# Kernel optimization log

Measured on AMD Instinct MI355X. Metric: run time of the kernel, lower is better.

Reference implementation:

```python
import jax, jax.numpy as jnp
import numpy as np

HEADS = 24
HEAD_DIM = 128
HIDDEN = HEADS * HEAD_DIM          # 3072
MLP_DIM = int(HIDDEN * 4.0)        # 12288
EPS = 1e-6


def _layernorm(x, eps=EPS):
    mu = jnp.mean(x, axis=-1, keepdims=True)
    var = jnp.mean(jnp.square(x - mu), axis=-1, keepdims=True)
    return (x - mu) * jax.lax.rsqrt(var + eps)


def _rmsnorm(x, w, eps=EPS):
    var = jnp.mean(jnp.square(x), axis=-1, keepdims=True)
    return x * jax.lax.rsqrt(var + eps) * w


def _apply_rope_transposed(x, freqs_cis):
    # x: [B, S_img, H, Dh]; freqs_cis: [S_img, 2*Dh]
    cos, sin = jnp.split(freqs_cis[:, None, :], 2, axis=-1)  # each [S_img, 1, Dh]
    xr = x.reshape(*x.shape[:-1], -1, 2)                      # interleaved pairs
    x_real, x_imag = xr[..., 0], xr[..., 1]
    x_rot = jnp.stack([-x_imag, x_real], axis=-1).reshape(x.shape)
    return x * cos + x_rot * sin


def setup_inputs() -> dict:
    key = jax.random.key(0)
    ks = jax.random.split(key, 20)
    B, S_IMG, S_TXT = 1, 2048, 256
    s = 0.02
    inp = {
        "hidden_states": jax.random.normal(ks[0], (B, S_IMG, HIDDEN), jnp.float32),
        "encoder_hidden_states": jax.random.normal(ks[1], (B, S_TXT, HIDDEN), jnp.float32),
        "temb": jax.random.normal(ks[2], (B, HIDDEN), jnp.float32),
        "freqs_cis": jax.random.uniform(ks[3], (S_IMG, 2 * HEAD_DIM), jnp.float32),
        # AdaLN: Linear(hidden, 3*hidden)
        "w_norm": jax.random.normal(ks[4], (HIDDEN, 3 * HIDDEN), jnp.float32) * s,
        "b_norm": jnp.zeros((3 * HIDDEN,), jnp.float32),
        # attention projections (bias=True)
        "wq": jax.random.normal(ks[5], (HIDDEN, HIDDEN), jnp.float32) * s,
        "bq": jnp.zeros((HIDDEN,), jnp.float32),
        "wk": jax.random.normal(ks[6], (HIDDEN, HIDDEN), jnp.float32) * s,
        "bk": jnp.zeros((HIDDEN,), jnp.float32),
        "wv": jax.random.normal(ks[7], (HIDDEN, HIDDEN), jnp.float32) * s,
        "bv": jnp.zeros((HIDDEN,), jnp.float32),
        # QK RMSNorm weights over head_dim
        "nq_w": jnp.ones((HEAD_DIM,), jnp.float32),
        "nk_w": jnp.ones((HEAD_DIM,), jnp.float32),
        # parallel MLP branch
        "w_mlp": jax.random.normal(ks[8], (HIDDEN, MLP_DIM), jnp.float32) * s,
        "b_mlp": jnp.zeros((MLP_DIM,), jnp.float32),
        # proj_out: Linear(hidden + mlp_dim, hidden)
        "w_out": jax.random.normal(ks[9], (HIDDEN + MLP_DIM, HIDDEN), jnp.float32) * s,
        "b_out": jnp.zeros((HIDDEN,), jnp.float32),
    }
    return inp


def reference(hidden_states, encoder_hidden_states, temb, freqs_cis,
              w_norm, b_norm, wq, bq, wk, bk, wv, bv, nq_w, nk_w,
              w_mlp, b_mlp, w_out, b_out):
    B = hidden_states.shape[0]
    T = encoder_hidden_states.shape[1]  # text_seq_length

    x = jnp.concatenate([hidden_states, encoder_hidden_states], axis=1)  # [B,S,D]
    residual = x

    # AdaLayerNormZeroSingle
    emb = jax.nn.silu(temb) @ w_norm + b_norm          # [B, 3D]
    emb = emb[:, None, :]                              # [B, 1, 3D]
    shift, scale, gate = jnp.split(emb, 3, axis=-1)    # each [B,1,D]
    nx = _layernorm(x) * (1.0 + scale) + shift         # [B,S,D]

    # parallel MLP branch
    mlp = jax.nn.gelu(nx @ w_mlp + b_mlp, approximate=True)  # [B,S,MLP]

    # attention: q/k/v over full (img+txt) normed sequence
    q = (nx @ wq + bq).reshape(B, -1, HEADS, HEAD_DIM)
    k = (nx @ wk + bk).reshape(B, -1, HEADS, HEAD_DIM)
    v = (nx @ wv + bv).reshape(B, -1, HEADS, HEAD_DIM)
    q = _rmsnorm(q, nq_w)
    k = _rmsnorm(k, nk_w)

    # transposed RoPE on image tokens only
    q = jnp.concatenate([_apply_rope_transposed(q[:, :-T], freqs_cis), q[:, -T:]], axis=1)
    k = jnp.concatenate([_apply_rope_transposed(k[:, :-T], freqs_cis), k[:, -T:]], axis=1)

    # full (non-varlen) scaled dot-product attention
    scores = jnp.einsum("bqhd,bkhd->bhqk", q, k) / np.sqrt(HEAD_DIM).astype(np.float32)
    probs = jax.nn.softmax(scores, axis=-1)
    attn = jnp.einsum("bhqk,bkhd->bqhd", probs, v).reshape(B, -1, HIDDEN)

    # concat attention + mlp, project, gated residual
    h = jnp.concatenate([attn, mlp], axis=2)           # [B,S,D+MLP]
    h = gate * (h @ w_out + b_out) + residual          # [B,S,D]

    return h[:, :-T, :], h[:, -T:, :]
```

## Files before the change

### kernel.cpp

```cpp
#include <hip/hip_runtime.h>
#include <hip/hip_bf16.h>

typedef unsigned short u16;
typedef short s16x8 __attribute__((ext_vector_type(8)));
typedef float f32x4 __attribute__((ext_vector_type(4)));
typedef int   i32x4 __attribute__((ext_vector_type(4)));
typedef int   i32x2 __attribute__((ext_vector_type(2)));
typedef u16   u16x4 __attribute__((ext_vector_type(4)));
typedef unsigned int u32;
typedef u32   u32x2 __attribute__((ext_vector_type(2)));

#define HEADS  24
#define HD     128
#define HIDDEN 3072
#define MLPD   12288
#define NTOK   2304
#define SIMG   2048
#define NEMB   9216
#define CATD   15360
#define QKVD   9216
#define FUSEN  21504
#define LN_EPS 1e-6f
#define MB     9
#define INV127SQ (1.0f/16129.0f)

__device__ __forceinline__ u16 f2us(float f){
  __hip_bfloat16 h = __float2bfloat16(f);
  return *reinterpret_cast<u16*>(&h);
}
__device__ __forceinline__ float us2f(u16 u){
  __hip_bfloat16 h;
  *reinterpret_cast<u16*>(&h) = u;
  return __bfloat162float(h);
}
__device__ __forceinline__ float gelu_tanh(float x){
  float y = 0.7978845608028654f*(x + 0.044715f*x*x*x);
  y = fminf(fmaxf(y, -12.f), 12.f);
  float e = __expf(-2.f*y);
  float t = (1.f - e) / (1.f + e);
  return 0.5f*x*(1.0f + t);
}
__device__ __forceinline__ int q8i(float x, float s){
  int q = __float2int_rn(x*s);
  return max(-127, min(127, q));
}
__device__ __forceinline__ void gload16(const void* g, void* l){
  __builtin_amdgcn_global_load_lds(
      (const __attribute__((address_space(1))) void*)g,
      (__attribute__((address_space(3))) void*)l, 16, 0, 0);
}
#define BAR() do{ asm volatile("":::"memory"); __builtin_amdgcn_s_barrier(); asm volatile("":::"memory"); }while(0)
#define LGKM0() asm volatile("s_waitcnt lgkmcnt(0)":::"memory")
#define VMW_(n) asm volatile("s_waitcnt vmcnt(" #n ")":::"memory")
#define VMW(n) VMW_(n)

__global__ __launch_bounds__(256)
void emb_partial(const float* __restrict__ temb, const float* __restrict__ wn,
                 float* __restrict__ partial)
{
  __shared__ float ls[384];
  int tid = threadIdx.x;
  int kb = blockIdx.y * 384;
  for (int i = tid; i < 384; i += 256){
    float t = temb[kb + i];
    ls[i] = t / (1.0f + __expf(-t));
  }
  __syncthreads();
  int j = blockIdx.x*256 + tid;
  const float* wp = wn + (size_t)kb*NEMB + j;
  float acc = 0.f;
  #pragma unroll 8
  for (int i = 0; i < 384; i++){ acc = fmaf(ls[i], wp[0], acc); wp += NEMB; }
  partial[blockIdx.y*NEMB + j] = acc;
}

__global__ __launch_bounds__(256)
void emb_reduce(const float* __restrict__ partial, const float* __restrict__ bn,
                float* __restrict__ emb)
{
  int j = blockIdx.x*256 + threadIdx.x;
  float s = bn[j];
  #pragma unroll
  for (int r = 0; r < 8; r++) s += partial[r*NEMB + j];
  emb[j] = s;
}

__global__ __launch_bounds__(256)
void ln_mod(const float* __restrict__ hs, const float* __restrict__ ehs,
            const float* __restrict__ emb, char* __restrict__ nx,
            float* __restrict__ arow)
{
  int row = blockIdx.x;
  const float* x = (row < SIMG) ? hs + (size_t)row*HIDDEN
                                : ehs + (size_t)(row - SIMG)*HIDDEN;
  int tid = threadIdx.x;
  float vals[12];
  float s = 0.f, ss = 0.f;
  #pragma unroll
  for (int i = 0; i < 3; i++){
    float4 v = *reinterpret_cast<const float4*>(x + i*1024 + tid*4);
    vals[i*4+0]=v.x; vals[i*4+1]=v.y; vals[i*4+2]=v.z; vals[i*4+3]=v.w;
    s += v.x+v.y+v.z+v.w;
    ss += v.x*v.x + v.y*v.y + v.z*v.z + v.w*v.w;
  }
  #pragma unroll
  for (int d = 1; d < 64; d <<= 1){ s += __shfl_xor(s, d); ss += __shfl_xor(ss, d); }
  __shared__ float red[8];
  if ((tid & 63) == 0){ red[tid>>6] = s; red[4 + (tid>>6)] = ss; }
  __syncthreads();
  s  = red[0]+red[1]+red[2]+red[3];
  ss = red[4]+red[5]+red[6]+red[7];
  float mu = s * (1.0f/HIDDEN);
  float var = ss * (1.0f/HIDDEN) - mu*mu;
  float rs = rsqrtf(var + LN_EPS);

  float mx = 1e-8f;
  #pragma unroll
  for (int i = 0; i < 3; i++){
    int col = i*1024 + tid*4;
    #pragma unroll
    for (int j = 0; j < 4; j++){
      float nv = (vals[i*4+j] - mu) * rs;
      float outv = nv * (1.0f + emb[HIDDEN + col + j]) + emb[col + j];
      vals[i*4+j] = outv;
      mx = fmaxf(mx, fabsf(outv));
    }
  }
  #pragma unroll
  for (int d = 1; d < 64; d <<= 1) mx = fmaxf(mx, __shfl_xor(mx, d));
  __shared__ float redm[4];
  if ((tid & 63) == 0) redm[tid>>6] = mx;
  __syncthreads();
  mx = fmaxf(fmaxf(redm[0], redm[1]), fmaxf(redm[2], redm[3]));
  if (tid == 0) arow[row] = mx;
  float sq = 127.0f / mx;

  #pragma unroll
  for (int i = 0; i < 3; i++){
    int col = i*1024 + tid*4;
    u32 pk = 0;
    #pragma unroll
    for (int j = 0; j < 4; j++)
      pk |= ((u32)(unsigned char)(char)q8i(vals[i*4+j], sq)) << (8*j);
    *reinterpret_cast<u32*>(nx + (size_t)row*HIDDEN + col) = pk;
  }
}

__global__ __launch_bounds__(256)
void wcolmax_atomic(const float* __restrict__ W, u32* __restrict__ wcol,
                    int N, int noff)
{
  int n = blockIdx.x*256 + threadIdx.x;
  const float* p = W + (size_t)blockIdx.y*64*N + n;
  float m = 0.f;
  #pragma unroll 8
  for (int k = 0; k < 64; k++){ m = fmaxf(m, fabsf(*p)); p += N; }
  atomicMax(wcol + noff + n, __float_as_uint(m));
}

__global__ __launch_bounds__(256)
void transpose_w_i8(const float* __restrict__ W, char* __restrict__ Wt,
                    int K, int N, int ldt, int noff,
                    const float* __restrict__ wcol)
{
  __shared__ float t[64][65];
  const int tid = threadIdx.x;
  const int kb = blockIdx.y * 64, nb = blockIdx.x * 64;
  #pragma unroll
  for (int i = 0; i < 4; i++){
    int row = (tid >> 4) + i*16;
    int c4  = (tid & 15) * 4;
    float4 v = *reinterpret_cast<const float4*>(W + (size_t)(kb+row)*N + nb + c4);
    t[row][c4] = v.x; t[row][c4+1] = v.y; t[row][c4+2] = v.z; t[row][c4+3] = v.w;
  }
  __syncthreads();
  int n  = tid >> 2;
  int kc = (tid & 3) * 16;
  float sq = 127.0f / fmaxf(wcol[noff + nb + n], 1e-8f);
  u32 w0=0,w1=0,w2=0,w3=0;
  #pragma unroll
  for (int j = 0; j < 4; j++)  w0 |= ((u32)(unsigned char)(char)q8i(t[kc+j][n],    sq)) << (8*j);
  #pragma unroll
  for (int j = 0; j < 4; j++)  w1 |= ((u32)(unsigned char)(char)q8i(t[kc+4+j][n],  sq)) << (8*j);
  #pragma unroll
  for (int j = 0; j < 4; j++)  w2 |= ((u32)(unsigned char)(char)q8i(t[kc+8+j][n],  sq)) << (8*j);
  #pragma unroll
  for (int j = 0; j < 4; j++)  w3 |= ((u32)(unsigned char)(char)q8i(t[kc+12+j][n], sq)) << (8*j);
  i32x4 o; o[0]=(int)w0; o[1]=(int)w1; o[2]=(int)w2; o[3]=(int)w3;
  *reinterpret_cast<i32x4*>(Wt + (size_t)(noff + nb + n)*ldt + kb + kc) = o;
}

__global__ __launch_bounds__(256)
void transpose_w(const float* __restrict__ W, u16* __restrict__ Wt,
                 int K, int N, int ldt, int noff)
{
  __shared__ float t[64][65];
  const int tid = threadIdx.x;
  const int kb = blockIdx.y * 64, nb = blockIdx.x * 64;
  #pragma unroll
  for (int i = 0; i < 4; i++){
    int row = (tid >> 4) + i*16;
    int c4  = (tid & 15) * 4;
    float4 v = *reinterpret_cast<const float4*>(W + (size_t)(kb+row)*N + nb + c4);
    t[row][c4] = v.x; t[row][c4+1] = v.y; t[row][c4+2] = v.z; t[row][c4+3] = v.w;
  }
  __syncthreads();
  int n  = tid >> 2;
  int kc = (tid & 3) * 16;
  u16 tmp[16];
  #pragma unroll
  for (int j = 0; j < 16; j++) tmp[j] = f2us(t[kc+j][n]);
  u16* dst = Wt + (size_t)(noff + nb + n)*ldt + kb + kc;
  *reinterpret_cast<i32x4*>(dst)     = *reinterpret_cast<const i32x4*>(tmp);
  *reinterpret_cast<i32x4*>(dst + 8) = *reinterpret_cast<const i32x4*>(tmp + 8);
}

__global__ __launch_bounds__(512, 2)
void gemm_i8(const char* __restrict__ A_, int lda,
             const char* __restrict__ Bt_, int ldb,
             const float* __restrict__ arow, const float* __restrict__ wcol,
             const float* __restrict__ b0, const float* __restrict__ b1,
             const float* __restrict__ b2, const float* __restrict__ b3,
             u16* __restrict__ qkvo, u16* __restrict__ hcat)
{
  extern __shared__ __align__(16) char ldsc[];
  const int tid = threadIdx.x, lane = tid & 63, wid = tid >> 6;
  const int l15 = lane & 15, lhi = lane >> 4;
  const int wm = wid >> 2, wn = wid & 3;
  const int NT = HIDDEN / 64;

  const int nwg = gridDim.x;
  int orig = blockIdx.x;
  int qq = nwg >> 3, rr = nwg & 7;
  int xcd = orig & 7, loc = orig >> 3;
  int wg = (xcd < rr ? xcd*(qq+1) : rr*(qq+1) + (xcd-rr)*qq) + loc;
  const int m0 = (wg % MB) * 256;
  const int n0 = (wg / MB) * 256;

  const char *gAlo, *gAhi, *gBlo, *gBhi;
  {
    int r  = tid >> 3;
    int g  = (tid & 7) ^ (r & 7);
    int R  = 2*r + (g >> 2);
    int j  = g & 3;
    gAlo = A_  + (size_t)(m0 + R)*lda + j*16;
    gAhi = A_  + (size_t)(m0 + 128 + R)*lda + j*16;
    gBlo = Bt_ + (size_t)(n0 + R)*ldb + j*16;
    gBhi = Bt_ + (size_t)(n0 + 128 + R)*ldb + j*16;
  }
  char* dst16 = ldsc + tid*16;

  const char *paw, *pbw;
  {
    int Ra = wm*128 + l15;
    paw = ldsc + (Ra>>1)*128 + (((((Ra&1)<<2)|lhi) ^ ((Ra>>1)&7))*16);
    int Rb = wn*64 + l15;
    pbw = ldsc + 49152 + (Rb>>1)*128 + (((((Rb&1)<<2)|lhi) ^ ((Rb>>1)&7))*16);
  }

  i32x4 acc[8][4];
  #pragma unroll
  for (int i = 0; i < 8; i++)
    #pragma unroll
    for (int j = 0; j < 4; j++){ i32x4 z = {0,0,0,0}; acc[i][j] = z; }

  #define PRIO1() __builtin_amdgcn_s_setprio(1)
  #define PRIO0() __builtin_amdgcn_s_setprio(0)

  #define TILE_I8(P_,DOI_,DOV_,GOFF_) do{                                      \
    constexpr int PS_ = ((P_)+2)%3;                                            \
    i32x4 aset[8], bset[4];                                                    \
    _Pragma("unroll") for (int i_=0;i_<4;i_++)                                 \
      aset[i_] = *reinterpret_cast<const i32x4*>(paw + (P_)*16384 + i_*1024);  \
    _Pragma("unroll") for (int i_=0;i_<4;i_++)                                 \
      bset[i_] = *reinterpret_cast<const i32x4*>(pbw + (P_)*16384 + i_*1024);  \
    _Pragma("unroll") for (int i_=0;i_<4;i_++)                                 \
      aset[4+i_] = *reinterpret_cast<const i32x4*>(paw + (P_)*16384 + 4096 + i_*1024);\
    if (DOI_){                                                                 \
      gload16(gAlo+(GOFF_), dst16 + PS_*16384);                                \
      gload16(gAhi+(GOFF_), dst16 + PS_*16384 + 8192);                         \
      gload16(gBlo+(GOFF_), dst16 + 49152 + PS_*16384);                        \
      gload16(gBhi+(GOFF_), dst16 + 49152 + PS_*16384 + 8192);                 \
    }                                                                          \
    PRIO1();                                                                   \
    _Pragma("unroll") for (int q_=0;q_<2;q_++)                                 \
      _Pragma("unroll") for (int h_=0;h_<2;h_++)                               \
        _Pragma("unroll") for (int mf_=0;mf_<4;mf_++)                          \
          _Pragma("unroll") for (int nf_=0;nf_<2;nf_++)                        \
            acc[q_*4+mf_][h_*2+nf_] = __builtin_amdgcn_mfma_i32_16x16x64_i8(   \
                aset[q_*4+mf_], bset[h_*2+nf_], acc[q_*4+mf_][h_*2+nf_],0,0,0);\
    PRIO0();                                                                   \
    LGKM0();                                                                   \
    if ((DOV_)==1) VMW(4);                                                     \
    if ((DOV_)==2) VMW(0);                                                     \
    BAR();                                                                     \
  }while(0)

  gload16(gAlo,    dst16);          gload16(gAhi,    dst16 + 8192);
  gload16(gBlo,    dst16 + 49152);  gload16(gBhi,    dst16 + 57344);
  gload16(gAlo+64, dst16 + 16384);  gload16(gAhi+64, dst16 + 24576);
  gload16(gBlo+64, dst16 + 65536);  gload16(gBhi+64, dst16 + 73728);
  VMW(4);
  BAR();

  for (int m = 0; m < NT/3 - 1; m++){
    TILE_I8(0,1,1,128);
    TILE_I8(1,1,1,192);
    TILE_I8(2,1,1,256);
    gAlo += 192; gAhi += 192; gBlo += 192; gBhi += 192;
  }
  TILE_I8(0,1,1,128);
  TILE_I8(1,0,2,0);
  TILE_I8(2,0,0,0);

  #undef TILE_I8
  #undef PRIO1
  #undef PRIO0

  #pragma unroll
  for (int a = 0; a < 8; a++){
    #pragma unroll
    for (int nf = 0; nf < 4; nf++){
      int col = n0 + wn*64 + nf*16 + l15;
      float wsc = wcol[col] * INV127SQ;
      #pragma unroll
      for (int r = 0; r < 4; r++){
        int row = m0 + wm*128 + a*16 + lhi*4 + r;
        float v = (float)acc[a][nf][r] * arow[row] * wsc;
        if (col < QKVD){
          const float* bp = b0; int c = col;
          if (c >= 6144){ bp = b2; c -= 6144; }
          else if (c >= 3072){ bp = b1; c -= 3072; }
          qkvo[(size_t)row*QKVD + col] = f2us(v + bp[c]);
        } else {
          int c2 = col - QKVD;
          hcat[(size_t)row*CATD + HIDDEN + c2] = f2us(gelu_tanh(v + b3[c2]));
        }
      }
    }
  }
}

__global__ __launch_bounds__(512, 2)
void gemm8(const u16* __restrict__ A_, int lda,
           const u16* __restrict__ Bt_, int ldb,
           int K, int N, int kspl,
           float* __restrict__ outf)
{
  extern __shared__ __align__(16) u16 lds[];
  const int tid = threadIdx.x, lane = tid & 63, wid = tid >> 6;
  const int l15 = lane & 15, lhi = lane >> 4;
  const int wm = wid >> 2, wn = wid & 3;
  const int NKH = K / 32;

  const u16* Ag = A_  + (size_t)blockIdx.z * kspl;
  const u16* Bg = Bt_ + (size_t)blockIdx.z * kspl;

  const int nwg = gridDim.x;
  int orig = blockIdx.x;
  int qq = nwg >> 3, rr = nwg & 7;
  int xcd = orig & 7, loc = orig >> 3;
  int wg = (xcd < rr ? xcd*(qq+1) : rr*(qq+1) + (xcd-rr)*qq) + loc;
  const int m0 = (wg % MB) * 256;
  const int n0 = (wg / MB) * 256;

  const u16 *gA0, *gA1, *gB0, *gB1;
  {
    size_t offA[2], offB[2];
    #pragma unroll
    for (int q = 0; q < 2; q++){
      int Lb = q*8192 + tid*16;
      int r  = Lb >> 7;
      int gp = (Lb >> 4) & 7;
      int g  = gp ^ (r & 7);
      int row = 2*r + (g >> 2);
      int ke  = (g & 3) * 8;
      offA[q] = (size_t)(m0 + row)*lda + ke;
      offB[q] = (size_t)(n0 + row)*ldb + ke;
    }
    gA0 = Ag + offA[0]; gA1 = Ag + offA[1];
    gB0 = Bg + offB[0]; gB1 = Bg + offB[1];
  }
  u16* dA0 = lds + tid*8;
  u16* dA1 = lds + 4096 + tid*8;
  u16* dB0 = lds + 32768 + tid*8;
  u16* dB1 = lds + 36864 + tid*8;

  const char *pa0, *pb0;
  {
    const char* LB = (const char*)lds;
    int Ra = wm*128 + l15;
    pa0 = LB + (Ra>>1)*128 + (((((Ra&1)<<2)|lhi) ^ ((Ra>>1)&7))*16);
    int Rb = wn*64 + l15;
    pb0 = LB + 65536 + (Rb>>1)*128 + (((((Rb&1)<<2)|lhi) ^ ((Rb>>1)&7))*16);
  }

  f32x4 acc[8][4];
  #pragma unroll
  for (int i = 0; i < 8; i++)
    #pragma unroll
    for (int j = 0; j < 4; j++){ f32x4 z = {0.f,0.f,0.f,0.f}; acc[i][j] = z; }

  #define LD8(P_) (*reinterpret_cast<const s16x8*>(P_))
  #define MFMA_ALL(AF_, BF_) do{                                               \
    _Pragma("unroll") for (int a_=0;a_<8;a_++)                                 \
      _Pragma("unroll") for (int nf_=0;nf_<4;nf_++)                            \
        acc[a_][nf_] = __builtin_amdgcn_mfma_f32_16x16x32_bf16(                \
            (AF_)[a_], (BF_)[nf_], acc[a_][nf_], 0, 0, 0); }while(0)

  #define PHASEP(RP_,SP_,DOI_,GOFF_,VN_) do{                                   \
    s16x8 af[8], bf[4];                                                        \
    af[0] = LD8(pa0 + (RP_)*16384);                                            \
    _Pragma("unroll") for (int i_=0;i_<4;i_++)                                 \
      bf[i_] = LD8(pb0 + (RP_)*16384 + i_*1024);                               \
    _Pragma("unroll") for (int i_=1;i_<8;i_++)                                 \
      af[i_] = LD8(pa0 + (RP_)*16384 + (i_>>2)*4096 + (i_&3)*1024);            \
    if (DOI_){                                                                 \
      gload16(gA0+(GOFF_), dA0+(SP_)*8192); gload16(gA1+(GOFF_), dA1+(SP_)*8192);\
      gload16(gB0+(GOFF_), dB0+(SP_)*8192); gload16(gB1+(GOFF_), dB1+(SP_)*8192);\
    }                                                                          \
    __builtin_amdgcn_s_setprio(1);                                             \
    MFMA_ALL(af, bf);                                                          \
    __builtin_amdgcn_s_setprio(0);                                             \
    LGKM0();                                                                   \
    VMW(VN_);                                                                  \
    BAR();                                                                     \
  }while(0)

  gload16(gA0,    dA0);        gload16(gA1,    dA1);
  gload16(gB0,    dB0);        gload16(gB1,    dB1);
  gload16(gA0+32, dA0+8192);   gload16(gA1+32, dA1+8192);
  gload16(gB0+32, dB0+8192);   gload16(gB1+32, dB1+8192);
  gload16(gA0+64, dA0+16384);  gload16(gA1+64, dA1+16384);
  gload16(gB0+64, dB0+16384);  gload16(gB1+64, dB1+16384);
  VMW(8);
  BAR();

  const int nblk = NKH >> 3;
  for (int b = 0; b < nblk - 1; b++){
    PHASEP(0,3,1, 96,8); PHASEP(1,0,1,128,8); PHASEP(2,1,1,160,8); PHASEP(3,2,1,192,8);
    PHASEP(0,3,1,224,8); PHASEP(1,0,1,256,8); PHASEP(2,1,1,288,8); PHASEP(3,2,1,320,8);
    gA0 += 256; gA1 += 256; gB0 += 256; gB1 += 256;
  }
  PHASEP(0,3,1, 96,8); PHASEP(1,0,1,128,8); PHASEP(2,1,1,160,8); PHASEP(3,2,1,192,8);
  PHASEP(0,3,1,224,8); PHASEP(1,0,0,  0,4); PHASEP(2,1,0,  0,0); PHASEP(3,2,0,  0,0);

  #undef PHASEP
  #undef MFMA_ALL
  #undef LD8

  #pragma unroll
  for (int a = 0; a < 8; a++){
    #pragma unroll
    for (int nf = 0; nf < 4; nf++){
      int col = n0 + wn*64 + nf*16 + l15;
      #pragma unroll
      for (int r = 0; r < 4; r++){
        int row = m0 + wm*128 + a*16 + lhi*4 + r;
        outf[(size_t)blockIdx.z*NTOK*HIDDEN + (size_t)row*HIDDEN + col] = acc[a][nf][r];
      }
    }
  }
}

__global__ __launch_bounds__(256)
void reduce_out(const float* __restrict__ part, const float* __restrict__ bout,
                const float* __restrict__ emb,
                const float* __restrict__ hs, const float* __restrict__ ehs,
                float* __restrict__ outp)
{
  int row = blockIdx.x;
  const float* res = (row < SIMG) ? hs + (size_t)row*HIDDEN
                                  : ehs + (size_t)(row - SIMG)*HIDDEN;
  #pragma unroll
  for (int i = 0; i < 3; i++){
    int col = i*1024 + threadIdx.x*4;
    float4 a = *reinterpret_cast<const float4*>(part + (size_t)row*HIDDEN + col);
    float4 b = *reinterpret_cast<const float4*>(part + (size_t)NTOK*HIDDEN + (size_t)row*HIDDEN + col);
    float4 rr = *reinterpret_cast<const float4*>(res + col);
    float4 bb = *reinterpret_cast<const float4*>(bout + col);
    float4 gg = *reinterpret_cast<const float4*>(emb + 2*HIDDEN + col);
    float4 o;
    o.x = gg.x*(a.x+b.x+bb.x) + rr.x;
    o.y = gg.y*(a.y+b.y+bb.y) + rr.y;
    o.z = gg.z*(a.z+b.z+bb.z) + rr.z;
    o.w = gg.w*(a.w+b.w+bb.w) + rr.w;
    *reinterpret_cast<float4*>(outp + (size_t)row*HIDDEN + col) = o;
  }
}

__global__ __launch_bounds__(256)
void qk_post(u16* __restrict__ qkv,
             const float* __restrict__ nqw, const float* __restrict__ nkw,
             const float* __restrict__ fc)
{
  int rid = blockIdx.x*4 + (threadIdx.x >> 6);
  int lane = threadIdx.x & 63;
  int isK = rid >= NTOK*HEADS;
  int r = isK ? rid - NTOK*HEADS : rid;
  int token = r / HEADS, head = r % HEADS;
  u16* p = qkv + (size_t)token*QKVD + (isK ? HIDDEN : 0) + head*HD + lane*2;
  unsigned int u = *reinterpret_cast<unsigned int*>(p);
  float v0 = us2f((u16)(u & 0xffff));
  float v1 = us2f((u16)(u >> 16));
  float ss = v0*v0 + v1*v1;
  #pragma unroll
  for (int d = 1; d < 64; d <<= 1) ss += __shfl_xor(ss, d);
  float rs = rsqrtf(ss * (1.0f/HD) + LN_EPS);
  const float* wv = isK ? nkw : nqw;
  v0 *= rs * wv[lane*2];
  v1 *= rs * wv[lane*2+1];
  if (token < SIMG){
    const float* f = fc + (size_t)token*(2*HD);
    float c0 = f[lane*2],      c1 = f[lane*2+1];
    float s0 = f[HD + lane*2], s1 = f[HD + lane*2+1];
    float o0 = v0*c0 - v1*s0;
    float o1 = v1*c1 + v0*s1;
    v0 = o0; v1 = o1;
  }
  unsigned int uo = (unsigned int)f2us(v0) | ((unsigned int)f2us(v1) << 16);
  *reinterpret_cast<unsigned int*>(p) = uo;
}

__global__ __launch_bounds__(512)
void attn_kernel(const u16* __restrict__ qkv, u16* __restrict__ hcat)
{
  __shared__ __align__(16) u16 Ks[64][136];
  __shared__ __align__(16) u16 Vt[128][72];
  __shared__ __align__(16) u16 Ps[128][72];

  const int tid = threadIdx.x, lane = tid & 63, w = tid >> 6;
  const int head = blockIdx.y;
  const int l15 = lane & 15, lhi = lane >> 4;
  const int q0 = blockIdx.x * 128;
  const float scale = 0.08838834764831845f;

  s16x8 qf[4];
  {
    const u16* qrow = qkv + (size_t)(q0 + w*16 + l15)*QKVD + head*HD;
    #pragma unroll
    for (int ks = 0; ks < 4; ks++)
      qf[ks] = *reinterpret_cast<const s16x8*>(qrow + ks*32 + lhi*8);
  }

  int krow[2], kd0[2];
  #pragma unroll
  for (int i = 0; i < 2; i++){ int c = tid + 512*i; krow[i] = c >> 4; kd0[i] = (c & 15)*8; }
  const int vd0   = (tid & 31) * 4;
  const int vbase = (tid >> 5) * 4;
  char* vwp = (char*)(&Vt[0][0]) + vd0*144 + (((vbase>>3) ^ ((vd0>>3)&7))*16) + (vbase&7)*2;

  i32x4 kr0, kr1;
  i32x2 vr0, vr1, vr2, vr3;
  {
    const u16* kbp = qkv + HIDDEN + (size_t)head*HD;
    const u16* vbp = qkv + 2*HIDDEN + (size_t)head*HD;
    kr0 = *reinterpret_cast<const i32x4*>(kbp + (size_t)(krow[0])*QKVD + kd0[0]);
    kr1 = *reinterpret_cast<const i32x4*>(kbp + (size_t)(krow[1])*QKVD + kd0[1]);
    vr0 = *reinterpret_cast<const i32x2*>(vbp + (size_t)(vbase+0)*QKVD + vd0);
    vr1 = *reinterpret_cast<const i32x2*>(vbp + (size_t)(vbase+1)*QKVD + vd0);
    vr2 = *reinterpret_cast<const i32x2*>(vbp + (size_t)(vbase+2)*QKVD + vd0);
    vr3 = *reinterpret_cast<const i32x2*>(vbp + (size_t)(vbase+3)*QKVD + vd0);
  }

  f32x4 O[8];
  #pragma unroll
  for (int i = 0; i < 8; i++){ f32x4 z = {0.f,0.f,0.f,0.f}; O[i] = z; }
  float mrow[4], lrow[4];
  #pragma unroll
  for (int r = 0; r < 4; r++){ mrow[r] = -1e30f; lrow[r] = 0.f; }

  for (int kv0 = 0; kv0 < NTOK; kv0 += 64){
    *reinterpret_cast<i32x4*>(&Ks[krow[0]][kd0[0]]) = kr0;
    *reinterpret_cast<i32x4*>(&Ks[krow[1]][kd0[1]]) = kr1;
    #pragma unroll
    for (int dd = 0; dd < 4; dd++){
      u32 a0 = (u32)(dd & 1 ? ((u32)vr0[dd>>1]) >> 16 : ((u32)vr0[dd>>1]) & 0xffff);
      u32 a1 = (u32)(dd & 1 ? ((u32)vr1[dd>>1]) >> 16 : ((u32)vr1[dd>>1]) & 0xffff);
      u32 a2 = (u32)(dd & 1 ? ((u32)vr2[dd>>1]) >> 16 : ((u32)vr2[dd>>1]) & 0xffff);
      u32 a3 = (u32)(dd & 1 ? ((u32)vr3[dd>>1]) >> 16 : ((u32)vr3[dd>>1]) & 0xffff);
      u32x2 pk; pk[0] = a0 | (a1 << 16); pk[1] = a2 | (a3 << 16);
      *reinterpret_cast<u32x2*>(vwp + dd*144) = pk;
    }
    __syncthreads();

    if (kv0 + 64 < NTOK){
      const u16* kbp = qkv + (size_t)(kv0+64)*QKVD + HIDDEN + (size_t)head*HD;
      const u16* vbp = qkv + (size_t)(kv0+64)*QKVD + 2*HIDDEN + (size_t)head*HD;
      kr0 = *reinterpret_cast<const i32x4*>(kbp + (size_t)(krow[0])*QKVD + kd0[0]);
      kr1 = *reinterpret_cast<const i32x4*>(kbp + (size_t)(krow[1])*QKVD + kd0[1]);
      vr0 = *reinterpret_cast<const i32x2*>(vbp + (size_t)(vbase+0)*QKVD + vd0);
      vr1 = *reinterpret_cast<const i32x2*>(vbp + (size_t)(vbase+1)*QKVD + vd0);
      vr2 = *reinterpret_cast<const i32x2*>(vbp + (size_t)(vbase+2)*QKVD + vd0);
      vr3 = *reinterpret_cast<const i32x2*>(vbp + (size_t)(vbase+3)*QKVD + vd0);
    }

    f32x4 S[4];
    #pragma unroll
    for (int nf = 0; nf < 4; nf++){ f32x4 z = {0.f,0.f,0.f,0.f}; S[nf] = z; }
    #pragma unroll
    for (int ks = 0; ks < 4; ks++){
      #pragma unroll
      for (int nf = 0; nf < 4; nf++){
        s16x8 b = *reinterpret_cast<const s16x8*>(&Ks[nf*16 + l15][ks*32 + lhi*8]);
        S[nf] = __builtin_amdgcn_mfma_f32_16x16x32_bf16(qf[ks], b, S[nf], 0, 0, 0);
      }
    }
    #pragma unroll
    for (int nf = 0; nf < 4; nf++)
      #pragma unroll
      for (int r = 0; r < 4; r++) S[nf][r] *= scale;

    float fsc[4];
    #pragma unroll
    for (int r = 0; r < 4; r++){
      float mx = -1e30f;
      #pragma unroll
      for (int nf = 0; nf < 4; nf++) mx = fmaxf(mx, S[nf][r]);
      #pragma unroll
      for (int d = 1; d < 16; d <<= 1) mx = fmaxf(mx, __shfl_xor(mx, d));
      float mn = fmaxf(mrow[r], mx);
      float f = __expf(mrow[r] - mn);
      mrow[r] = mn; fsc[r] = f;
      float lsum = 0.f;
      int prow = w*16 + lhi*4 + r;
      #pragma unroll
      for (int nf = 0; nf < 4; nf++){
        float pvl = __expf(S[nf][r] - mn);
        lsum += pvl;
        int pcol = nf*16 + l15;
        int col = (((pcol>>3) ^ (prow&7)) << 3) | (pcol & 7);
        Ps[prow][col] = f2us(pvl);
      }
      #pragma unroll
      for (int d = 1; d < 16; d <<= 1) lsum += __shfl_xor(lsum, d);
      lrow[r] = lrow[r]*f + lsum;
    }
    #pragma unroll
    for (int nf = 0; nf < 8; nf++)
      #pragma unroll
      for (int r = 0; r < 4; r++) O[nf][r] *= fsc[r];

    #pragma unroll
    for (int ks = 0; ks < 2; ks++){
      int prow = w*16 + l15;
      int cb = ((ks*4 + lhi) ^ (prow & 7)) << 3;
      s16x8 a = *reinterpret_cast<const s16x8*>(&Ps[prow][cb]);
      #pragma unroll
      for (int nf = 0; nf < 8; nf++){
        int d = nf*16 + l15;
        int vb = ((ks*4 + lhi) ^ ((d>>3)&7)) << 3;
        s16x8 b = *reinterpret_cast<const s16x8*>(&Vt[d][vb]);
        O[nf] = __builtin_amdgcn_mfma_f32_16x16x32_bf16(a, b, O[nf], 0, 0, 0);
      }
    }
    __syncthreads();
  }

  #pragma unroll
  for (int nf = 0; nf < 8; nf++){
    #pragma unroll
    for (int r = 0; r < 4; r++){
      int row = q0 + w*16 + lhi*4 + r;
      int col = head*HD + nf*16 + l15;
      hcat[(size_t)row*CATD + col] = f2us(O[nf][r] / lrow[r]);
    }
  }
}

extern "C" void kernel_launch(void* const* d_in, const int* in_sizes, int n_in,
                              void* d_out, int out_size, void* d_ws, size_t ws_size,
                              hipStream_t stream)
{
  const float* hs    = (const float*)d_in[0];
  const float* ehs   = (const float*)d_in[1];
  const float* temb  = (const float*)d_in[2];
  const float* fc    = (const float*)d_in[3];
  const float* wnorm = (const float*)d_in[4];
  const float* bnorm = (const float*)d_in[5];
  const float* wq    = (const float*)d_in[6];
  const float* bq    = (const float*)d_in[7];
  const float* wk    = (const float*)d_in[8];
  const float* bk    = (const float*)d_in[9];
  const float* wv    = (const float*)d_in[10];
  const float* bv    = (const float*)d_in[11];
  const float* nqw   = (const float*)d_in[12];
  const float* nkw   = (const float*)d_in[13];
  const float* wmlp  = (const float*)d_in[14];
  const float* bmlp  = (const float*)d_in[15];
  const float* wout  = (const float*)d_in[16];
  const float* bout  = (const float*)d_in[17];
  float* outp = (float*)d_out;

  char* ws = (char*)d_ws;
  float* emb   = (float*)ws;
  float* part  = (float*)(ws + 36864);
  float* arow  = (float*)(ws + 331776);
  u32*   wcol  = (u32*)(ws + 340992);
  char*  nx8   = ws + 771072;
  u16*   qkv   = (u16*)(ws + 7848960);
  u16*   hcat  = (u16*)(ws + 57394176);
  char*  wreg  = ws + 128173056;
  char*  wt8   = wreg;
  u16*   wtb   = (u16*)wreg;
  float* partial = (float*)nx8;

  hipFuncSetAttribute((const void*)gemm_i8, hipFuncAttributeMaxDynamicSharedMemorySize, 98304);
  hipFuncSetAttribute((const void*)gemm8,   hipFuncAttributeMaxDynamicSharedMemorySize, 131072);

  emb_partial<<<dim3(36,8), 256, 0, stream>>>(temb, wnorm, part);
  emb_reduce<<<36, 256, 0, stream>>>(part, bnorm, emb);
  ln_mod<<<NTOK, 256, 0, stream>>>(hs, ehs, emb, nx8, arow);

  hipMemsetAsync(wcol, 0, FUSEN*4, stream);
  wcolmax_atomic<<<dim3(12,48), 256, 0, stream>>>(wq,   wcol, HIDDEN, 0);
  wcolmax_atomic<<<dim3(12,48), 256, 0, stream>>>(wk,   wcol, HIDDEN, HIDDEN);
  wcolmax_atomic<<<dim3(12,48), 256, 0, stream>>>(wv,   wcol, HIDDEN, 2*HIDDEN);
  wcolmax_atomic<<<dim3(48,48), 256, 0, stream>>>(wmlp, wcol, MLPD, QKVD);

  transpose_w_i8<<<dim3(48,48), 256, 0, stream>>>(wq,   wt8, HIDDEN, HIDDEN, HIDDEN, 0,        (const float*)wcol);
  transpose_w_i8<<<dim3(48,48), 256, 0, stream>>>(wk,   wt8, HIDDEN, HIDDEN, HIDDEN, HIDDEN,   (const float*)wcol);
  transpose_w_i8<<<dim3(48,48), 256, 0, stream>>>(wv,   wt8, HIDDEN, HIDDEN, HIDDEN, 2*HIDDEN, (const float*)wcol);
  transpose_w_i8<<<dim3(192,48), 256, 0, stream>>>(wmlp, wt8, HIDDEN, MLPD, HIDDEN, QKVD,      (const float*)wcol);

  gemm_i8<<<dim3((FUSEN/256)*MB, 1, 1), 512, 98304, stream>>>(
      nx8, HIDDEN, wt8, HIDDEN, arow, (const float*)wcol, bq, bk, bv, bmlp, qkv, hcat);

  transpose_w<<<dim3(48,240), 256, 0, stream>>>(wout, wtb, CATD, HIDDEN, CATD, 0);

  qk_post<<<(2*NTOK*HEADS)/4, 256, 0, stream>>>(qkv, nqw, nkw, fc);
  attn_kernel<<<dim3(NTOK/128, HEADS), 512, 0, stream>>>(qkv, hcat);

  gemm8<<<dim3((HIDDEN/256)*MB, 1, 2), 512, 131072, stream>>>(
      hcat, CATD, wtb, CATD, CATD/2, HIDDEN, CATD/2, partial);

  reduce_out<<<NTOK, 256, 0, stream>>>(partial, bout, emb, hs, ehs, outp);
}
```

Baseline: 900.5 us.

## Merge weight prep launches, split emb GEMV wider, skip redundant softmax rescale

The per-matrix colmax and int8 transpose kernels for wq/wk/wv/wmlp are merged into single launches that pick the source matrix from the global column index. This cuts launch count and the tail gaps between small grids. The temb GEMV is split across 16 K-chunks instead of 8 to put more blocks in flight, and the workspace offsets are moved to fit the larger partial buffer. In attention, the online-softmax rescale of O and l only runs when any row max in the wavefront increases, which saves exp and multiply work at the cost of a wave-wide vote.

```diff
diff --git a/kernel.cpp b/kernel.cpp
--- a/kernel.cpp
+++ b/kernel.cpp
@@ -58,19 +58,19 @@
 void emb_partial(const float* __restrict__ temb, const float* __restrict__ wn,
                  float* __restrict__ partial)
 {
-  __shared__ float ls[384];
+  __shared__ float ls[192];
   int tid = threadIdx.x;
-  int kb = blockIdx.y * 384;
-  for (int i = tid; i < 384; i += 256){
-    float t = temb[kb + i];
-    ls[i] = t / (1.0f + __expf(-t));
+  int kb = blockIdx.y * 192;
+  if (tid < 192){
+    float t = temb[kb + tid];
+    ls[tid] = t / (1.0f + __expf(-t));
   }
   __syncthreads();
   int j = blockIdx.x*256 + tid;
   const float* wp = wn + (size_t)kb*NEMB + j;
   float acc = 0.f;
   #pragma unroll 8
-  for (int i = 0; i < 384; i++){ acc = fmaf(ls[i], wp[0], acc); wp += NEMB; }
+  for (int i = 0; i < 192; i++){ acc = fmaf(ls[i], wp[0], acc); wp += NEMB; }
   partial[blockIdx.y*NEMB + j] = acc;
 }
 
@@ -81,7 +81,7 @@
   int j = blockIdx.x*256 + threadIdx.x;
   float s = bn[j];
   #pragma unroll
-  for (int r = 0; r < 8; r++) s += partial[r*NEMB + j];
+  for (int r = 0; r < 16; r++) s += partial[r*NEMB + j];
   emb[j] = s;
 }
 
@@ -147,36 +147,53 @@
 }
 
 __global__ __launch_bounds__(256)
-void wcolmax_atomic(const float* __restrict__ W, u32* __restrict__ wcol,
-                    int N, int noff)
-{
-  int n = blockIdx.x*256 + threadIdx.x;
+void wcolmax_all(const float* __restrict__ wq, const float* __restrict__ wk,
+                 const float* __restrict__ wv, const float* __restrict__ wmlp,
+                 u32* __restrict__ wcol)
+{
+  int gcol = blockIdx.x*256 + threadIdx.x;
+  const float* W; int n, N;
+  if (gcol < QKVD){
+    int m = gcol / HIDDEN;
+    W = (m == 0) ? wq : (m == 1 ? wk : wv);
+    n = gcol % HIDDEN; N = HIDDEN;
+  } else {
+    W = wmlp; n = gcol - QKVD; N = MLPD;
+  }
   const float* p = W + (size_t)blockIdx.y*64*N + n;
   float m = 0.f;
   #pragma unroll 8
   for (int k = 0; k < 64; k++){ m = fmaxf(m, fabsf(*p)); p += N; }
-  atomicMax(wcol + noff + n, __float_as_uint(m));
+  atomicMax(wcol + gcol, __float_as_uint(m));
 }
 
 __global__ __launch_bounds__(256)
-void transpose_w_i8(const float* __restrict__ W, char* __restrict__ Wt,
-                    int K, int N, int ldt, int noff,
-                    const float* __restrict__ wcol)
+void transpose_w_i8_all(const float* __restrict__ wq, const float* __restrict__ wk,
+                        const float* __restrict__ wv, const float* __restrict__ wmlp,
+                        char* __restrict__ Wt, const float* __restrict__ wcol)
 {
   __shared__ float t[64][65];
   const int tid = threadIdx.x;
-  const int kb = blockIdx.y * 64, nb = blockIdx.x * 64;
+  const int gnb = blockIdx.x * 64, kb = blockIdx.y * 64;
+  const float* W; int N, nbl;
+  if (gnb < QKVD){
+    int m = gnb / HIDDEN;
+    W = (m == 0) ? wq : (m == 1 ? wk : wv);
+    N = HIDDEN; nbl = gnb % HIDDEN;
+  } else {
+    W = wmlp; N = MLPD; nbl = gnb - QKVD;
+  }
   #pragma unroll
   for (int i = 0; i < 4; i++){
     int row = (tid >> 4) + i*16;
     int c4  = (tid & 15) * 4;
-    float4 v = *reinterpret_cast<const float4*>(W + (size_t)(kb+row)*N + nb + c4);
+    float4 v = *reinterpret_cast<const float4*>(W + (size_t)(kb+row)*N + nbl + c4);
     t[row][c4] = v.x; t[row][c4+1] = v.y; t[row][c4+2] = v.z; t[row][c4+3] = v.w;
   }
   __syncthreads();
   int n  = tid >> 2;
   int kc = (tid & 3) * 16;
-  float sq = 127.0f / fmaxf(wcol[noff + nb + n], 1e-8f);
+  float sq = 127.0f / fmaxf(wcol[gnb + n], 1e-8f);
   u32 w0=0,w1=0,w2=0,w3=0;
   #pragma unroll
   for (int j = 0; j < 4; j++)  w0 |= ((u32)(unsigned char)(char)q8i(t[kc+j][n],    sq)) << (8*j);
@@ -187,7 +204,7 @@
   #pragma unroll
   for (int j = 0; j < 4; j++)  w3 |= ((u32)(unsigned char)(char)q8i(t[kc+12+j][n], sq)) << (8*j);
   i32x4 o; o[0]=(int)w0; o[1]=(int)w1; o[2]=(int)w2; o[3]=(int)w3;
-  *reinterpret_cast<i32x4*>(Wt + (size_t)(noff + nb + n)*ldt + kb + kc) = o;
+  *reinterpret_cast<i32x4*>(Wt + (size_t)(gnb + n)*HIDDEN + kb + kc) = o;
 }
 
 __global__ __launch_bounds__(256)
@@ -611,7 +628,7 @@
       #pragma unroll
       for (int r = 0; r < 4; r++) S[nf][r] *= scale;
 
-    float fsc[4];
+    float pmax[4];
     #pragma unroll
     for (int r = 0; r < 4; r++){
       float mx = -1e30f;
@@ -619,14 +636,34 @@
       for (int nf = 0; nf < 4; nf++) mx = fmaxf(mx, S[nf][r]);
       #pragma unroll
       for (int d = 1; d < 16; d <<= 1) mx = fmaxf(mx, __shfl_xor(mx, d));
-      float mn = fmaxf(mrow[r], mx);
-      float f = __expf(mrow[r] - mn);
-      mrow[r] = mn; fsc[r] = f;
+      pmax[r] = mx;
+    }
+    bool need = false;
+    #pragma unroll
+    for (int r = 0; r < 4; r++) need = need || (pmax[r] > mrow[r]);
+    if (__any(need)){
+      float fsc[4];
+      #pragma unroll
+      for (int r = 0; r < 4; r++){
+        float mn = fmaxf(mrow[r], pmax[r]);
+        fsc[r] = __expf(mrow[r] - mn);
+        mrow[r] = mn;
+      }
+      #pragma unroll
+      for (int nf = 0; nf < 8; nf++)
+        #pragma unroll
+        for (int r = 0; r < 4; r++) O[nf][r] *= fsc[r];
+      #pragma unroll
+      for (int r = 0; r < 4; r++) lrow[r] *= fsc[r];
+    }
+
+    #pragma unroll
+    for (int r = 0; r < 4; r++){
       float lsum = 0.f;
       int prow = w*16 + lhi*4 + r;
       #pragma unroll
       for (int nf = 0; nf < 4; nf++){
-        float pvl = __expf(S[nf][r] - mn);
+        float pvl = __expf(S[nf][r] - mrow[r]);
         lsum += pvl;
         int pcol = nf*16 + l15;
         int col = (((pcol>>3) ^ (prow&7)) << 3) | (pcol & 7);
@@ -634,12 +671,8 @@
       }
       #pragma unroll
       for (int d = 1; d < 16; d <<= 1) lsum += __shfl_xor(lsum, d);
-      lrow[r] = lrow[r]*f + lsum;
-    }
-    #pragma unroll
-    for (int nf = 0; nf < 8; nf++)
-      #pragma unroll
-      for (int r = 0; r < 4; r++) O[nf][r] *= fsc[r];
+      lrow[r] += lsum;
+    }
 
     #pragma unroll
     for (int ks = 0; ks < 2; ks++){
@@ -695,8 +728,8 @@
   char* ws = (char*)d_ws;
   float* emb   = (float*)ws;
   float* part  = (float*)(ws + 36864);
-  float* arow  = (float*)(ws + 331776);
-  u32*   wcol  = (u32*)(ws + 340992);
+  float* arow  = (float*)(ws + 626688);
+  u32*   wcol  = (u32*)(ws + 635904);
   char*  nx8   = ws + 771072;
   u16*   qkv   = (u16*)(ws + 7848960);
   u16*   hcat  = (u16*)(ws + 57394176);
@@ -708,20 +741,15 @@
   hipFuncSetAttribute((const void*)gemm_i8, hipFuncAttributeMaxDynamicSharedMemorySize, 98304);
   hipFuncSetAttribute((const void*)gemm8,   hipFuncAttributeMaxDynamicSharedMemorySize, 131072);
 
-  emb_partial<<<dim3(36,8), 256, 0, stream>>>(temb, wnorm, part);
+  emb_partial<<<dim3(36,16), 256, 0, stream>>>(temb, wnorm, part);
   emb_reduce<<<36, 256, 0, stream>>>(part, bnorm, emb);
   ln_mod<<<NTOK, 256, 0, stream>>>(hs, ehs, emb, nx8, arow);
 
   hipMemsetAsync(wcol, 0, FUSEN*4, stream);
-  wcolmax_atomic<<<dim3(12,48), 256, 0, stream>>>(wq,   wcol, HIDDEN, 0);
-  wcolmax_atomic<<<dim3(12,48), 256, 0, stream>>>(wk,   wcol, HIDDEN, HIDDEN);
-  wcolmax_atomic<<<dim3(12,48), 256, 0, stream>>>(wv,   wcol, HIDDEN, 2*HIDDEN);
-  wcolmax_atomic<<<dim3(48,48), 256, 0, stream>>>(wmlp, wcol, MLPD, QKVD);
-
-  transpose_w_i8<<<dim3(48,48), 256, 0, stream>>>(wq,   wt8, HIDDEN, HIDDEN, HIDDEN, 0,        (const float*)wcol);
-  transpose_w_i8<<<dim3(48,48), 256, 0, stream>>>(wk,   wt8, HIDDEN, HIDDEN, HIDDEN, HIDDEN,   (const float*)wcol);
-  transpose_w_i8<<<dim3(48,48), 256, 0, stream>>>(wv,   wt8, HIDDEN, HIDDEN, HIDDEN, 2*HIDDEN, (const float*)wcol);
-  transpose_w_i8<<<dim3(192,48), 256, 0, stream>>>(wmlp, wt8, HIDDEN, MLPD, HIDDEN, QKVD,      (const float*)wcol);
+  wcolmax_all<<<dim3(FUSEN/256, 48), 256, 0, stream>>>(wq, wk, wv, wmlp, wcol);
+
+  transpose_w_i8_all<<<dim3(FUSEN/64, 48), 256, 0, stream>>>(
+      wq, wk, wv, wmlp, wt8, (const float*)wcol);
 
   gemm_i8<<<dim3((FUSEN/256)*MB, 1, 1), 512, 98304, stream>>>(
       nx8, HIDDEN, wt8, HIDDEN, arow, (const float*)wcol, bq, bk, bv, bmlp, qkv, hcat);
```

Result: faster. 876.2 us (-2.7%).
